# Kernel optimization log

Measured on AMD Instinct MI355X. Metric: run time of the kernel, lower is better.

Reference implementation:

```python
import jax, jax.numpy as jnp
import numpy as np

B, N, D, H = 8, 1024, 768, 12
HD = D // H  # 64


def setup_inputs() -> dict:
    key = jax.random.key(0)
    ks = jax.random.split(key, 10)
    input_graph = jax.random.normal(ks[0], (B, N, D), dtype=jnp.float32)
    u = jax.random.uniform(ks[1], (B, N, N), dtype=jnp.float32)
    keep = jax.random.uniform(ks[2], (B, N, N)) < 0.15
    adj = jnp.where(keep, u, 0.0)
    s = 1.0 / np.sqrt(D)
    Wq = jax.random.normal(ks[3], (D, D), dtype=jnp.float32) * s
    bq = jnp.zeros((D,), dtype=jnp.float32)
    Wk = jax.random.normal(ks[4], (D, D), dtype=jnp.float32) * s
    bk = jnp.zeros((D,), dtype=jnp.float32)
    Wv = jax.random.normal(ks[5], (D, D), dtype=jnp.float32) * s
    bv = jnp.zeros((D,), dtype=jnp.float32)
    beta = jnp.asarray(0.1, dtype=jnp.float32)
    return {"input_graph": input_graph, "adj": adj, "Wq": Wq, "bq": bq,
            "Wk": Wk, "bk": bk, "Wv": Wv, "bv": bv, "beta": beta}


def _split_heads(x):
    # [B,N,D] -> [B,H,N,HD]
    b, n, _ = x.shape
    return x.reshape(b, n, H, HD).transpose(0, 2, 1, 3)


def reference(input_graph, adj, Wq, bq, Wk, bk, Wv, bv, beta):
    q = _split_heads(input_graph @ Wq + bq)  # [B,H,N,HD]
    k = _split_heads(input_graph @ Wk + bk)
    v = _split_heads(input_graph @ Wv + bv)
    scores = jnp.einsum('bhqd,bhkd->bhqk', q, k) / jnp.sqrt(jnp.asarray(HD, input_graph.dtype))
    adj_e = adj[:, None, :, :]  # [B,1,N,N]
    scores = scores + beta * adj_e
    scores = jnp.where(adj_e > 0, scores, jnp.asarray(-9e15, scores.dtype))
    probs = jax.nn.softmax(scores, axis=-1)
    out = jnp.einsum('bhqk,bhkd->bhqd', probs, v)  # [B,H,N,HD]
    return out.transpose(0, 2, 1, 3).reshape(input_graph.shape[0], input_graph.shape[1], D)
```

## Files before the change

kernel.cpp:

```cpp
#include <hip/hip_runtime.h>

#define B_ 8
#define N_ 1024
#define D_ 768
#define H_ 12
#define HD_ 64

#define LOG2E 1.4426950408889634f

typedef __attribute__((ext_vector_type(8))) short bf16x8;
typedef __attribute__((ext_vector_type(4))) short short4_t;
typedef __attribute__((ext_vector_type(4))) float f32x4;
typedef __attribute__((ext_vector_type(16))) float f32x16;
typedef unsigned int u32;

__device__ __forceinline__ short f2bf(float f) {
  union { float f; unsigned u; } v; v.f = f;
  unsigned u = v.u;
  unsigned r = u + 0x7fffu + ((u >> 16) & 1u);
  return (short)(r >> 16);
}
__device__ __forceinline__ float bf2f(short s) {
  union { unsigned u; float f; } v;
  v.u = ((unsigned)(unsigned short)s) << 16;
  return v.f;
}
__device__ __forceinline__ u32 cvtpk(float a, float b) {
  u32 r;
  asm("v_cvt_pk_bf16_f32 %0, %1, %2" : "=v"(r) : "v"(a), "v"(b));
  return r;
}
__device__ __forceinline__ void pl32swap(u32& a, u32& b) {
  asm("v_permlane32_swap_b32 %0, %1" : "+v"(a), "+v"(b));
}

__device__ __forceinline__ void gload_lds16(const void* g, void* l) {
  __builtin_amdgcn_global_load_lds((const __attribute__((address_space(1))) u32*)g,
                                   (__attribute__((address_space(3))) u32*)l, 16, 0, 0);
}

__global__ __launch_bounds__(256)
void cvt_kernel(const float* __restrict__ X, short* __restrict__ Xb,
                const float* __restrict__ Wq, const float* __restrict__ Wk,
                const float* __restrict__ Wv, short* __restrict__ Wt3) {
  const int bid = blockIdx.x;
  const int tid = threadIdx.x;

  if (bid < 3072) {
    int i = (bid * 256 + tid) * 8;
    float4 a = *(const float4*)(X + i);
    float4 b = *(const float4*)(X + i + 4);
    bf16x8 o;
    o[0] = f2bf(a.x); o[1] = f2bf(a.y); o[2] = f2bf(a.z); o[3] = f2bf(a.w);
    o[4] = f2bf(b.x); o[5] = f2bf(b.y); o[6] = f2bf(b.z); o[7] = f2bf(b.w);
    *(bf16x8*)(Xb + i) = o;
  } else {
    const int i = bid - 3072;
    const int z = i / 576;
    const int rem = i % 576;
    const int bx = rem % 24, by = rem / 24;
    const float* W = z == 0 ? Wq : (z == 1 ? Wk : Wv);
    short* O = Wt3 + (size_t)z * D_ * D_;
    __shared__ float t[32][33];
    const int n0 = bx * 32, k0 = by * 32;
    const int tx = tid & 31, ty = tid >> 5;
#pragma unroll
    for (int j = 0; j < 4; j++)
      t[ty + 8 * j][tx] = W[(size_t)(k0 + ty + 8 * j) * D_ + n0 + tx];
    __syncthreads();
#pragma unroll
    for (int j = 0; j < 4; j++)
      O[(size_t)(n0 + ty + 8 * j) * D_ + k0 + tx] = f2bf(t[tx][ty + 8 * j]);
  }
}

__global__ __launch_bounds__(256, 4)
void gemm_madj_kernel(const short* __restrict__ Xb, const short* __restrict__ Wt3,
                      const float* __restrict__ bq, const float* __restrict__ bk,
                      const float* __restrict__ bv, short* __restrict__ QKV,
                      const float* __restrict__ adj, const float* __restrict__ beta_p,
                      short* __restrict__ madjF) {
  __shared__ __align__(16) char smem[32768];
  const int bid = blockIdx.x;
  const int tid = threadIdx.x;

  if (bid < 1152) {
    const int z = bid / 384;
    const int n0 = ((bid >> 6) % 6) * 128;
    const int m0 = (bid & 63) * 128;
    const short* Wt = Wt3 + (size_t)z * D_ * D_;
    const float* bias = z == 0 ? bq : (z == 1 ? bk : bv);
    short* C = QKV + (size_t)z * (B_ * N_) * D_;
    const float alpha = (z == 0) ? 0.125f * LOG2E : 1.0f;

    const int lane = tid & 63;
    const int wid = tid >> 6;
    const int wr = (wid >> 1) * 64;
    const int wc = (wid & 1) * 64;
    const int l15 = lane & 15;
    const int lg = lane >> 4;

    short* At = (short*)smem;
    short* Bt = (short*)smem + 8192;

    f32x4 acc[4][4];
#pragma unroll
    for (int m = 0; m < 4; m++)
#pragma unroll
      for (int n = 0; n < 4; n++)
        acc[m][n] = (f32x4){0.f, 0.f, 0.f, 0.f};

    const int srow_l = lane >> 2;
    const int sc8 = (((lane & 3) ^ ((lane >> 2) & 3)) * 8);
    const short* ag = Xb + (size_t)(m0 + wid * 16 + srow_l) * D_ + sc8;
    const short* bg = Wt + (size_t)(n0 + wid * 16 + srow_l) * D_ + sc8;

    auto stage = [&](int bi, int k0) {
#pragma unroll
      for (int p = 0; p < 2; p++) {
        gload_lds16(ag + (size_t)(64 * p) * D_ + k0, At + bi * 4096 + (wid + 4 * p) * 512);
        gload_lds16(bg + (size_t)(64 * p) * D_ + k0, Bt + bi * 4096 + (wid + 4 * p) * 512);
      }
    };

    stage(0, 0);
    for (int k0 = 0; k0 < D_; k0 += 32) {
      const int cur = (k0 >> 5) & 1;
      __syncthreads();
      if (k0 + 32 < D_) stage(cur ^ 1, k0 + 32);

      bf16x8 af[4], bfr[4];
#pragma unroll
      for (int m = 0; m < 4; m++) {
        const int row = wr + m * 16 + l15;
        af[m] = *(const bf16x8*)(At + cur * 4096 + row * 32 + (lg ^ (l15 & 3)) * 8);
      }
#pragma unroll
      for (int n = 0; n < 4; n++) {
        const int row = wc + n * 16 + l15;
        bfr[n] = *(const bf16x8*)(Bt + cur * 4096 + row * 32 + (lg ^ (l15 & 3)) * 8);
      }
#pragma unroll
      for (int m = 0; m < 4; m++)
#pragma unroll
        for (int n = 0; n < 4; n++)
          acc[m][n] = __builtin_amdgcn_mfma_f32_16x16x32_bf16(af[m], bfr[n], acc[m][n], 0, 0, 0);
    }

    if (z == 2) {
#pragma unroll
      for (int n = 0; n < 4; n++) {
        const int col = n0 + wc + n * 16 + l15;
        const float bval = bias[col];
        const int hh = col >> 6, dd = col & 63;
#pragma unroll
        for (int m = 0; m < 4; m++) {
          const int row = m0 + wr + m * 16 + 4 * lg;
          const int bb = row >> 10, nn = row & 1023;
          short4_t o;
#pragma unroll
          for (int r = 0; r < 4; r++) o[r] = f2bf(acc[m][n][r] + bval);
          *(short4_t*)&C[(((size_t)bb * H_ + hh) * HD_ + dd) * N_ + nn] = o;
        }
      }
    } else {
#pragma unroll
      for (int n = 0; n < 4; n++) {
        const int col = n0 + wc + n * 16 + l15;
        const float bval = bias[col];
#pragma unroll
        for (int m = 0; m < 4; m++) {
#pragma unroll
          for (int r = 0; r < 4; r++) {
            const int row = m0 + wr + m * 16 + 4 * lg + r;
            C[(size_t)row * D_ + col] = f2bf((acc[m][n][r] + bval) * alpha);
          }
        }
      }
    }
  } else {
    const int j = bid - 1152;
    const int b = j >> 8;
    const int rr = j & 255;
    const int qt64 = rr >> 4, kt = rr & 15;
    const float b2 = beta_p[0] * LOG2E;
    const float MASKV = -9.0e15f * LOG2E;

    float* Lt = (float*)smem;
    {
      const int row = tid >> 2, cs = (tid & 3) * 16;
      const float* ap = adj + ((size_t)b * N_ + qt64 * 64 + row) * (size_t)N_ + kt * 64 + cs;
#pragma unroll
      for (int jj = 0; jj < 4; jj++)
        *(float4*)(Lt + row * 68 + cs + 4 * jj) = *(const float4*)(ap + 4 * jj);
    }
    __syncthreads();

    const int a = tid >> 1, cb = tid & 1;
    const int lane_att = a & 63;
    const int l31 = lane_att & 31, hia = lane_att >> 5;
    const int q_local = 32 * (a >> 6) + l31;

    short vals[16];
#pragma unroll
    for (int t = 0; t < 4; t++) {
      float4 a4 = *(const float4*)(Lt + q_local * 68 + 32 * cb + 8 * t + 4 * hia);
      float av[4] = {a4.x, a4.y, a4.z, a4.w};
#pragma unroll
      for (int r2 = 0; r2 < 4; r2++) {
        float av_ = av[r2];
        vals[4 * t + r2] = f2bf((av_ > 0.f) ? b2 * av_ : MASKV);
      }
    }
    short* o = madjF + ((size_t)((b * 8 + (qt64 >> 1)) * 16 + kt)) * 8192 +
               (qt64 & 1) * 4096 + tid * 16;
    bf16x8 lo, hi;
#pragma unroll
    for (int jj = 0; jj < 8; jj++) { lo[jj] = vals[jj]; hi[jj] = vals[8 + jj]; }
    *(bf16x8*)o = lo;
    *(bf16x8*)(o + 8) = hi;
  }
}

#define QK_HALF(SREG, K0, ROWOFF, MJA, MJB)                                    \
  {                                                                            \
    f32x16 c_;                                                                 \
    _Pragma("unroll") for (int r_ = 0; r_ < 8; r_++) c_[r_] = bf2f(MJA[r_]);   \
    _Pragma("unroll") for (int r_ = 0; r_ < 8; r_++) c_[8 + r_] = bf2f(MJB[r_]);\
    _Pragma("unroll") for (int s_ = 0; s_ < 4; s_++) {                         \
      bf16x8 kf_ = *(const bf16x8*)((K0) + ((ROWOFF) + l31) * 64 +             \
                                    (((2 * s_ + hi) ^ swz) * 8));              \
      c_ = __builtin_amdgcn_mfma_f32_32x32x16_bf16(kf_, qf[s_], c_, 0, 0, 0);  \
    }                                                                          \
    SREG = c_;                                                                 \
  }

#define PACK_HALF(SREG, FW, OFF)                                               \
  {                                                                            \
    _Pragma("unroll") for (int r_ = 0; r_ < 16; r_++) {                        \
      SREG[r_] = __builtin_exp2f(SREG[r_]); ps += SREG[r_];                    \
    }                                                                          \
    u32 wv_[8];                                                                \
    _Pragma("unroll") for (int c_ = 0; c_ < 8; c_++)                           \
      wv_[c_] = cvtpk(SREG[2 * c_], SREG[2 * c_ + 1]);                         \
    pl32swap(wv_[0], wv_[2]); FW[(OFF) + 0] = wv_[0]; FW[(OFF) + 2] = wv_[2];  \
    pl32swap(wv_[1], wv_[3]); FW[(OFF) + 1] = wv_[1]; FW[(OFF) + 3] = wv_[3];  \
    pl32swap(wv_[4], wv_[6]); FW[(OFF) + 4] = wv_[4]; FW[(OFF) + 6] = wv_[6];  \
    pl32swap(wv_[5], wv_[7]); FW[(OFF) + 5] = wv_[5]; FW[(OFF) + 7] = wv_[7];  \
  }

#define PV_HALF(FW, V0, KS0)                                                   \
  _Pragma("unroll") for (int ks_ = (KS0); ks_ < (KS0) + 2; ks_++) {            \
    union { u32 u[4]; bf16x8 v; } pu_;                                         \
    pu_.u[0] = FW[4 * ks_];     pu_.u[1] = FW[4 * ks_ + 1];                    \
    pu_.u[2] = FW[4 * ks_ + 2]; pu_.u[3] = FW[4 * ks_ + 3];                    \
    bf16x8 vf0_ = *(const bf16x8*)((V0) + l31 * 64 + (((2 * ks_ + hi) ^ swz) * 8)); \
    bf16x8 vf1_ = *(const bf16x8*)((V0) + (32 + l31) * 64 + (((2 * ks_ + hi) ^ swz) * 8)); \
    acc0 = __builtin_amdgcn_mfma_f32_32x32x16_bf16(vf0_, pu_.v, acc0, 0, 0, 0);\
    acc1 = __builtin_amdgcn_mfma_f32_32x32x16_bf16(vf1_, pu_.v, acc1, 0, 0, 0);\
  }

__global__ __launch_bounds__(256, 3)
void attn_kernel(const short* __restrict__ QKV, const short* __restrict__ madjF,
                 float* __restrict__ out) {
  const short* Qb = QKV;
  const short* Kb = QKV + (size_t)(B_ * N_) * D_;
  const short* VTg = QKV + 2 * (size_t)(B_ * N_) * D_;

  const int wg = blockIdx.x;
  const int b = wg & 7;
  const int rem = wg >> 3;
  const int h = rem >> 3;
  const int qt = rem & 7;

  const int tid = threadIdx.x;
  const int lane = tid & 63;
  const int w = tid >> 6;
  const int l31 = lane & 31;
  const int hi = lane >> 5;
  const int swz = lane & 7;

  const int q0 = qt * 128;
  const size_t seq0 = (size_t)b * N_;
  const int hc = h * HD_;

  __shared__ short Kt[2][64][64];
  __shared__ short VTt[3][64][64];

  bf16x8 qf[4];
  {
    const short* qp = Qb + (seq0 + q0 + 32 * w + l31) * (size_t)D_ + hc + 8 * hi;
#pragma unroll
    for (int s = 0; s < 4; s++) qf[s] = *(const bf16x8*)(qp + 16 * s);
  }

  f32x16 acc0 = {}, acc1 = {};
  float l_ = 0.f;

  const int srow = 16 * w + (lane >> 3);
  const int sc8 = ((lane & 7) ^ (lane >> 3)) * 8;
  const short* kg = Kb + (seq0 + srow) * (size_t)D_ + hc + sc8;
  const short* vg = VTg + ((size_t)(b * H_ + h) * HD_ + srow) * N_ + sc8;
  const short* mg = madjF + ((size_t)(b * 8 + qt) * 16) * 8192 + (w * 64 + lane) * 32;

  bf16x8 mjc[4], mjn[4];
  u32 fwP[16], fwN[16];

  {
    gload_lds16(kg, ((short*)Kt[0]) + (size_t)w * 1024);
    gload_lds16(kg + 8 * (size_t)D_, ((short*)Kt[0]) + (size_t)w * 1024 + 512);
    gload_lds16(vg, ((short*)VTt[0]) + (size_t)w * 1024);
    gload_lds16(vg + 8 * (size_t)N_, ((short*)VTt[0]) + (size_t)w * 1024 + 512);
#pragma unroll
    for (int j = 0; j < 4; j++) mjc[j] = *(const bf16x8*)(mg + 8 * j);
    __syncthreads();
    gload_lds16(kg + (size_t)64 * D_, ((short*)Kt[1]) + (size_t)w * 1024);
    gload_lds16(kg + (size_t)72 * D_, ((short*)Kt[1]) + (size_t)w * 1024 + 512);
    gload_lds16(vg + 64, ((short*)VTt[1]) + (size_t)w * 1024);
    gload_lds16(vg + 64 + 8 * (size_t)N_, ((short*)VTt[1]) + (size_t)w * 1024 + 512);
#pragma unroll
    for (int j = 0; j < 4; j++) mjn[j] = *(const bf16x8*)(mg + 8192 + 8 * j);

    float ps = 0.f;
    f32x16 s0, s1;
    const short* K0 = (const short*)Kt[0];
    QK_HALF(s0, K0, 0, mjc[0], mjc[1]);
    PACK_HALF(s0, fwP, 0);
    QK_HALF(s1, K0, 32, mjc[2], mjc[3]);
    PACK_HALF(s1, fwP, 8);
    l_ += ps;
#pragma unroll
    for (int j = 0; j < 4; j++) mjc[j] = mjn[j];
  }

  int vprev = 0;
  int vstage = 2;
  for (int t = 1; t < 16; t++) {
    __syncthreads();
    if (t < 15) {
      const int k0 = (t + 1) * 64;
      gload_lds16(kg + (size_t)k0 * D_, ((short*)Kt[(t + 1) & 1]) + (size_t)w * 1024);
      gload_lds16(kg + (size_t)(k0 + 8) * D_, ((short*)Kt[(t + 1) & 1]) + (size_t)w * 1024 + 512);
      gload_lds16(vg + k0, ((short*)VTt[vstage]) + (size_t)w * 1024);
      gload_lds16(vg + k0 + 8 * (size_t)N_, ((short*)VTt[vstage]) + (size_t)w * 1024 + 512);
#pragma unroll
      for (int j = 0; j < 4; j++)
        mjn[j] = *(const bf16x8*)(mg + (size_t)(t + 1) * 8192 + 8 * j);
    }

    const short* K0 = (const short*)Kt[t & 1];
    const short* V0 = (const short*)VTt[vprev];
    float ps = 0.f;
    f32x16 s0, s1;

    QK_HALF(s0, K0, 0, mjc[0], mjc[1]);
    PV_HALF(fwP, V0, 0);
    PACK_HALF(s0, fwN, 0);
    QK_HALF(s1, K0, 32, mjc[2], mjc[3]);
    PV_HALF(fwP, V0, 2);
    PACK_HALF(s1, fwN, 8);
    l_ += ps;

#pragma unroll
    for (int i = 0; i < 16; i++) fwP[i] = fwN[i];
#pragma unroll
    for (int j = 0; j < 4; j++) mjc[j] = mjn[j];
    vprev = (vprev == 2) ? 0 : vprev + 1;
    vstage = (vstage == 2) ? 0 : vstage + 1;
  }

  {
    const short* V0 = (const short*)VTt[vprev];
    PV_HALF(fwP, V0, 0);
    PV_HALF(fwP, V0, 2);
  }

  l_ += __shfl_xor(l_, 32);
  const float invl = 1.f / l_;
  float* orow = out + (seq0 + q0 + 32 * w + l31) * (size_t)D_ + hc;
#pragma unroll
  for (int t = 0; t < 4; t++) {
    float4 o0, o1;
    o0.x = acc0[4 * t] * invl;     o0.y = acc0[4 * t + 1] * invl;
    o0.z = acc0[4 * t + 2] * invl; o0.w = acc0[4 * t + 3] * invl;
    o1.x = acc1[4 * t] * invl;     o1.y = acc1[4 * t + 1] * invl;
    o1.z = acc1[4 * t + 2] * invl; o1.w = acc1[4 * t + 3] * invl;
    *(float4*)(orow + 8 * t + 4 * hi) = o0;
    *(float4*)(orow + 8 * t + 4 * hi + 32) = o1;
  }
}

extern "C" void kernel_launch(void* const* d_in, const int* in_sizes, int n_in,
                              void* d_out, int out_size, void* d_ws, size_t ws_size,
                              hipStream_t stream) {
  const float* X    = (const float*)d_in[0];
  const float* adj  = (const float*)d_in[1];
  const float* Wq   = (const float*)d_in[2];
  const float* bq   = (const float*)d_in[3];
  const float* Wk   = (const float*)d_in[4];
  const float* bk   = (const float*)d_in[5];
  const float* Wv   = (const float*)d_in[6];
  const float* bv   = (const float*)d_in[7];
  const float* beta = (const float*)d_in[8];
  float* out = (float*)d_out;

  short* Xb    = (short*)d_ws;
  short* Wt3   = Xb + (size_t)(B_ * N_) * D_;
  short* QKV   = Wt3 + 3 * (size_t)D_ * D_;
  short* madjF = QKV + 3 * (size_t)(B_ * N_) * D_;

  cvt_kernel<<<dim3(4800), 256, 0, stream>>>(X, Xb, Wq, Wk, Wv, Wt3);
  gemm_madj_kernel<<<dim3(3200), 256, 0, stream>>>(Xb, Wt3, bq, bk, bv, QKV, adj, beta, madjF);
  attn_kernel<<<dim3(768), 256, 0, stream>>>(QKV, madjF, out);
}
```

Before: 108.4 us.

## Load K/V tiles directly into registers, dropping LDS staging and barriers

Replaces the shared-memory double/triple-buffered K and V staging, and its per-tile __syncthreads, with direct global-to-register loads. Each wave fetches its own K and V^T fragments and prefetches the next tile's K and mask into a second register set, with the 16 tiles fully unrolled. The aim is to remove LDS traffic and block-wide barriers. In exchange, each of the 4 waves redundantly reads the same K/V from global/L2, register pressure rises, and the QK and PV overlap across tiles is lost.

Result: slower. 273.6 us (+152.3%).

```diff
diff --git a/kernel.cpp b/kernel.cpp
--- a/kernel.cpp
+++ b/kernel.cpp
@@ -222,19 +222,6 @@
   }
 }
 
-#define QK_HALF(SREG, K0, ROWOFF, MJA, MJB)                                    \
-  {                                                                            \
-    f32x16 c_;                                                                 \
-    _Pragma("unroll") for (int r_ = 0; r_ < 8; r_++) c_[r_] = bf2f(MJA[r_]);   \
-    _Pragma("unroll") for (int r_ = 0; r_ < 8; r_++) c_[8 + r_] = bf2f(MJB[r_]);\
-    _Pragma("unroll") for (int s_ = 0; s_ < 4; s_++) {                         \
-      bf16x8 kf_ = *(const bf16x8*)((K0) + ((ROWOFF) + l31) * 64 +             \
-                                    (((2 * s_ + hi) ^ swz) * 8));              \
-      c_ = __builtin_amdgcn_mfma_f32_32x32x16_bf16(kf_, qf[s_], c_, 0, 0, 0);  \
-    }                                                                          \
-    SREG = c_;                                                                 \
-  }
-
 #define PACK_HALF(SREG, FW, OFF)                                               \
   {                                                                            \
     _Pragma("unroll") for (int r_ = 0; r_ < 16; r_++) {                        \
@@ -249,15 +236,47 @@
     pl32swap(wv_[5], wv_[7]); FW[(OFF) + 5] = wv_[5]; FW[(OFF) + 7] = wv_[7];  \
   }
 
-#define PV_HALF(FW, V0, KS0)                                                   \
-  _Pragma("unroll") for (int ks_ = (KS0); ks_ < (KS0) + 2; ks_++) {            \
-    union { u32 u[4]; bf16x8 v; } pu_;                                         \
-    pu_.u[0] = FW[4 * ks_];     pu_.u[1] = FW[4 * ks_ + 1];                    \
-    pu_.u[2] = FW[4 * ks_ + 2]; pu_.u[3] = FW[4 * ks_ + 3];                    \
-    bf16x8 vf0_ = *(const bf16x8*)((V0) + l31 * 64 + (((2 * ks_ + hi) ^ swz) * 8)); \
-    bf16x8 vf1_ = *(const bf16x8*)((V0) + (32 + l31) * 64 + (((2 * ks_ + hi) ^ swz) * 8)); \
-    acc0 = __builtin_amdgcn_mfma_f32_32x32x16_bf16(vf0_, pu_.v, acc0, 0, 0, 0);\
-    acc1 = __builtin_amdgcn_mfma_f32_32x32x16_bf16(vf1_, pu_.v, acc1, 0, 0, 0);\
+#define ATTN_TILE(T, KVC, KVO, MJC, MJN, DO_NEXT)                              \
+  {                                                                            \
+    f32x16 s0_, s1_;                                                           \
+    {                                                                          \
+      f32x16 c_;                                                               \
+      _Pragma("unroll") for (int r_ = 0; r_ < 8; r_++) c_[r_] = bf2f(MJC[0][r_]);      \
+      _Pragma("unroll") for (int r_ = 0; r_ < 8; r_++) c_[8 + r_] = bf2f(MJC[1][r_]);  \
+      _Pragma("unroll") for (int s_ = 0; s_ < 4; s_++)                         \
+        c_ = __builtin_amdgcn_mfma_f32_32x32x16_bf16(KVC[s_], qf[s_], c_, 0, 0, 0);    \
+      s0_ = c_;                                                                \
+      _Pragma("unroll") for (int r_ = 0; r_ < 8; r_++) c_[r_] = bf2f(MJC[2][r_]);      \
+      _Pragma("unroll") for (int r_ = 0; r_ < 8; r_++) c_[8 + r_] = bf2f(MJC[3][r_]);  \
+      _Pragma("unroll") for (int s_ = 0; s_ < 4; s_++)                         \
+        c_ = __builtin_amdgcn_mfma_f32_32x32x16_bf16(KVC[4 + s_], qf[s_], c_, 0, 0, 0);\
+      s1_ = c_;                                                                \
+    }                                                                          \
+       \
+    _Pragma("unroll") for (int ks_ = 0; ks_ < 4; ks_++) {                      \
+      KVC[ks_]     = *(const bf16x8*)(vA_ + (size_t)(T) * 64 + 16 * ks_);      \
+      KVC[4 + ks_] = *(const bf16x8*)(vB_ + (size_t)(T) * 64 + 16 * ks_);      \
+    }                                                                          \
+    if (DO_NEXT) {                                                             \
+      _Pragma("unroll") for (int s_ = 0; s_ < 4; s_++) {                       \
+        KVO[s_]     = *(const bf16x8*)(kA_ + (size_t)((T) + 1) * 64 * D_ + 16 * s_);   \
+        KVO[4 + s_] = *(const bf16x8*)(kB_ + (size_t)((T) + 1) * 64 * D_ + 16 * s_);   \
+      }                                                                        \
+      _Pragma("unroll") for (int j_ = 0; j_ < 4; j_++)                         \
+        MJN[j_] = *(const bf16x8*)(mg + (size_t)((T) + 1) * 8192 + 8 * j_);    \
+    }                                                                          \
+    float ps = 0.f;                                                            \
+    u32 fw[16];                                                                \
+    PACK_HALF(s0_, fw, 0);                                                     \
+    PACK_HALF(s1_, fw, 8);                                                     \
+    l_ += ps;                                                                  \
+    _Pragma("unroll") for (int ks_ = 0; ks_ < 4; ks_++) {                      \
+      union { u32 u[4]; bf16x8 v; } pu_;                                       \
+      pu_.u[0] = fw[4 * ks_];     pu_.u[1] = fw[4 * ks_ + 1];                  \
+      pu_.u[2] = fw[4 * ks_ + 2]; pu_.u[3] = fw[4 * ks_ + 3];                  \
+      acc0 = __builtin_amdgcn_mfma_f32_32x32x16_bf16(KVC[ks_], pu_.v, acc0, 0, 0, 0);  \
+      acc1 = __builtin_amdgcn_mfma_f32_32x32x16_bf16(KVC[4 + ks_], pu_.v, acc1, 0, 0, 0); \
+    }                                                                          \
   }
 
 __global__ __launch_bounds__(256, 3)
@@ -278,15 +297,11 @@
   const int w = tid >> 6;
   const int l31 = lane & 31;
   const int hi = lane >> 5;
-  const int swz = lane & 7;
 
   const int q0 = qt * 128;
   const size_t seq0 = (size_t)b * N_;
   const int hc = h * HD_;
 
-  __shared__ short Kt[2][64][64];
-  __shared__ short VTt[3][64][64];
-
   bf16x8 qf[4];
   {
     const short* qp = Qb + (seq0 + q0 + 32 * w + l31) * (size_t)D_ + hc + 8 * hi;
@@ -297,83 +312,38 @@
   f32x16 acc0 = {}, acc1 = {};
   float l_ = 0.f;
 
-  const int srow = 16 * w + (lane >> 3);
-  const int sc8 = ((lane & 7) ^ (lane >> 3)) * 8;
-  const short* kg = Kb + (seq0 + srow) * (size_t)D_ + hc + sc8;
-  const short* vg = VTg + ((size_t)(b * H_ + h) * HD_ + srow) * N_ + sc8;
+  const short* kA_ = Kb + (seq0 + l31) * (size_t)D_ + hc + 8 * hi;
+  const short* kB_ = kA_ + (size_t)32 * D_;
+  const short* vA_ = VTg + ((size_t)(b * H_ + h) * HD_ + l31) * N_ + 8 * hi;
+  const short* vB_ = vA_ + (size_t)32 * N_;
   const short* mg = madjF + ((size_t)(b * 8 + qt) * 16) * 8192 + (w * 64 + lane) * 32;
 
-  bf16x8 mjc[4], mjn[4];
-  u32 fwP[16], fwN[16];
-
-  {
-    gload_lds16(kg, ((short*)Kt[0]) + (size_t)w * 1024);
-    gload_lds16(kg + 8 * (size_t)D_, ((short*)Kt[0]) + (size_t)w * 1024 + 512);
-    gload_lds16(vg, ((short*)VTt[0]) + (size_t)w * 1024);
-    gload_lds16(vg + 8 * (size_t)N_, ((short*)VTt[0]) + (size_t)w * 1024 + 512);
-#pragma unroll
-    for (int j = 0; j < 4; j++) mjc[j] = *(const bf16x8*)(mg + 8 * j);
-    __syncthreads();
-    gload_lds16(kg + (size_t)64 * D_, ((short*)Kt[1]) + (size_t)w * 1024);
-    gload_lds16(kg + (size_t)72 * D_, ((short*)Kt[1]) + (size_t)w * 1024 + 512);
-    gload_lds16(vg + 64, ((short*)VTt[1]) + (size_t)w * 1024);
-    gload_lds16(vg + 64 + 8 * (size_t)N_, ((short*)VTt[1]) + (size_t)w * 1024 + 512);
-#pragma unroll
-    for (int j = 0; j < 4; j++) mjn[j] = *(const bf16x8*)(mg + 8192 + 8 * j);
-
-    float ps = 0.f;
-    f32x16 s0, s1;
-    const short* K0 = (const short*)Kt[0];
-    QK_HALF(s0, K0, 0, mjc[0], mjc[1]);
-    PACK_HALF(s0, fwP, 0);
-    QK_HALF(s1, K0, 32, mjc[2], mjc[3]);
-    PACK_HALF(s1, fwP, 8);
-    l_ += ps;
-#pragma unroll
-    for (int j = 0; j < 4; j++) mjc[j] = mjn[j];
-  }
-
-  int vprev = 0;
-  int vstage = 2;
-  for (int t = 1; t < 16; t++) {
-    __syncthreads();
-    if (t < 15) {
-      const int k0 = (t + 1) * 64;
-      gload_lds16(kg + (size_t)k0 * D_, ((short*)Kt[(t + 1) & 1]) + (size_t)w * 1024);
-      gload_lds16(kg + (size_t)(k0 + 8) * D_, ((short*)Kt[(t + 1) & 1]) + (size_t)w * 1024 + 512);
-      gload_lds16(vg + k0, ((short*)VTt[vstage]) + (size_t)w * 1024);
-      gload_lds16(vg + k0 + 8 * (size_t)N_, ((short*)VTt[vstage]) + (size_t)w * 1024 + 512);
-#pragma unroll
-      for (int j = 0; j < 4; j++)
-        mjn[j] = *(const bf16x8*)(mg + (size_t)(t + 1) * 8192 + 8 * j);
-    }
-
-    const short* K0 = (const short*)Kt[t & 1];
-    const short* V0 = (const short*)VTt[vprev];
-    float ps = 0.f;
-    f32x16 s0, s1;
-
-    QK_HALF(s0, K0, 0, mjc[0], mjc[1]);
-    PV_HALF(fwP, V0, 0);
-    PACK_HALF(s0, fwN, 0);
-    QK_HALF(s1, K0, 32, mjc[2], mjc[3]);
-    PV_HALF(fwP, V0, 2);
-    PACK_HALF(s1, fwN, 8);
-    l_ += ps;
-
-#pragma unroll
-    for (int i = 0; i < 16; i++) fwP[i] = fwN[i];
-#pragma unroll
-    for (int j = 0; j < 4; j++) mjc[j] = mjn[j];
-    vprev = (vprev == 2) ? 0 : vprev + 1;
-    vstage = (vstage == 2) ? 0 : vstage + 1;
-  }
-
-  {
-    const short* V0 = (const short*)VTt[vprev];
-    PV_HALF(fwP, V0, 0);
-    PV_HALF(fwP, V0, 2);
-  }
+  bf16x8 kvA[8], kvB[8], mjA[4], mjB[4];
+
+#pragma unroll
+  for (int s = 0; s < 4; s++) {
+    kvA[s] = *(const bf16x8*)(kA_ + 16 * s);
+    kvA[4 + s] = *(const bf16x8*)(kB_ + 16 * s);
+  }
+#pragma unroll
+  for (int j = 0; j < 4; j++) mjA[j] = *(const bf16x8*)(mg + 8 * j);
+
+  ATTN_TILE(0,  kvA, kvB, mjA, mjB, 1)
+  ATTN_TILE(1,  kvB, kvA, mjB, mjA, 1)
+  ATTN_TILE(2,  kvA, kvB, mjA, mjB, 1)
+  ATTN_TILE(3,  kvB, kvA, mjB, mjA, 1)
+  ATTN_TILE(4,  kvA, kvB, mjA, mjB, 1)
+  ATTN_TILE(5,  kvB, kvA, mjB, mjA, 1)
+  ATTN_TILE(6,  kvA, kvB, mjA, mjB, 1)
+  ATTN_TILE(7,  kvB, kvA, mjB, mjA, 1)
+  ATTN_TILE(8,  kvA, kvB, mjA, mjB, 1)
+  ATTN_TILE(9,  kvB, kvA, mjB, mjA, 1)
+  ATTN_TILE(10, kvA, kvB, mjA, mjB, 1)
+  ATTN_TILE(11, kvB, kvA, mjB, mjA, 1)
+  ATTN_TILE(12, kvA, kvB, mjA, mjB, 1)
+  ATTN_TILE(13, kvB, kvA, mjB, mjA, 1)
+  ATTN_TILE(14, kvA, kvB, mjA, mjB, 1)
+  ATTN_TILE(15, kvB, kvA, mjB, mjA, 0)
 
   l_ += __shfl_xor(l_, 32);
   const float invl = 1.f / l_;
```
